# Performance work log

Measured on AMD Instinct MI355X. Metric: run time of the kernel, lower is better.

## Reference

```python
import jax, jax.numpy as jnp
import numpy as np
import math

B, SQ, SK, D = 32, 2048, 2048, 64


def setup_inputs() -> dict:
    key = jax.random.key(0)
    kq, kk, kv, km = jax.random.split(key, 4)
    Q = jax.random.normal(kq, (B, SQ, D), dtype=jnp.float32)
    K = jax.random.normal(kk, (B, SK, D), dtype=jnp.float32)
    V = jax.random.normal(kv, (B, SK, D), dtype=jnp.float32)
    mask = jax.random.randint(km, (B, SQ, SK), 0, 2) > 0  # bool, True = keep
    return {"Q": Q, "K": K, "V": V, "mask": mask}


def reference(Q, K, V, mask):
    dim_qk = Q.shape[-1]
    # [B, Sq, Sk] = Q @ K^T / sqrt(d)
    attn_score = jnp.einsum("bqd,bkd->bqk", Q, K) / math.sqrt(dim_qk)
    attn_score = jnp.where(mask, attn_score, jnp.float32(-1e9))
    attn_score = jax.nn.softmax(attn_score, axis=-1)
    output = jnp.einsum("bqk,bkd->bqd", attn_score, V)
    return (attn_score, output)
```

## Files before the change

kernel.cpp:

```cpp
#include <hip/hip_runtime.h>
#include <math.h>

#define NB 32
#define SQL 2048
#define SKL 2048
#define DH 64
#define EWP 40
#define SC 0.18033688011112042f

typedef __attribute__((ext_vector_type(8))) short short8;
typedef __attribute__((ext_vector_type(4))) float f32x4;
typedef __attribute__((ext_vector_type(4))) int   i32x4;
typedef __attribute__((ext_vector_type(2))) unsigned int u32x2;

__device__ __forceinline__ unsigned short f2bf(float f) {
    unsigned int u = __float_as_uint(f);
    u += 0x7FFFu + ((u >> 16) & 1u);
    return (unsigned short)(u >> 16);
}

__global__ __launch_bounds__(256)
void cvt_bf16_kernel(const float* __restrict__ in, unsigned short* __restrict__ out, int n4)
{
    const int i = blockIdx.x * 256 + threadIdx.x;
    if (i < n4) {
        const float4 v = reinterpret_cast<const float4*>(in)[i];
        ushort4 o;
        o.x = f2bf(v.x); o.y = f2bf(v.y); o.z = f2bf(v.z); o.w = f2bf(v.w);
        reinterpret_cast<ushort4*>(out)[i] = o;
    }
}

__global__ __launch_bounds__(256)
void vtrans_kernel(const float* __restrict__ V, unsigned short* __restrict__ Vt)
{
    __shared__ float tile[64][65];
    const int b  = blockIdx.x >> 5;
    const int kt = blockIdx.x & 31;
    const int t  = threadIdx.x;
    const int c4 = (t & 15) << 2;
    const int r0 = t >> 4;
    const float* vb = V + ((size_t)b * SKL + (size_t)kt * 64) * DH;
#pragma unroll
    for (int i = 0; i < 4; ++i) {
        const int r = r0 + i * 16;
        const float4 v = *reinterpret_cast<const float4*>(vb + (size_t)r * DH + c4);
        tile[r][c4] = v.x; tile[r][c4 + 1] = v.y; tile[r][c4 + 2] = v.z; tile[r][c4 + 3] = v.w;
    }
    __syncthreads();
    unsigned short* ob = Vt + (size_t)b * DH * SKL + (size_t)kt * 64;
#pragma unroll
    for (int i = 0; i < 4; ++i) {
        const int d = r0 + i * 16;
        ushort4 o;
        o.x = f2bf(tile[c4 + 0][d]);
        o.y = f2bf(tile[c4 + 1][d]);
        o.z = f2bf(tile[c4 + 2][d]);
        o.w = f2bf(tile[c4 + 3][d]);
        *reinterpret_cast<ushort4*>(ob + (size_t)d * SKL + c4) = o;
    }
}

__global__ __launch_bounds__(256, 6)
void sdpa_mfma_kernel(const unsigned short* __restrict__ Qb,
                      const unsigned short* __restrict__ Kb,
                      const unsigned short* __restrict__ Vtb,
                      const int* __restrict__ Mp,
                      float* __restrict__ Pout, float* __restrict__ Oout)
{
    __shared__ float ored[4][16][68];
    __shared__ float l_part[4][16];
    __shared__ float inv_l[16];

    const int tid  = threadIdx.x;
    const int w    = tid >> 6;
    const int lane = tid & 63;
    const int quad = lane >> 4;
    const int s    = lane & 15;
    const int b    = blockIdx.x >> 7;
    const int qt   = blockIdx.x & 127;
    const int g0   = (b << 11) + (qt << 4);

    const unsigned short* qrow = Qb + (size_t)(g0 + s) * DH + quad * 8;
    const short8 aq0 = *reinterpret_cast<const short8*>(qrow);
    const short8 aq1 = *reinterpret_cast<const short8*>(qrow + 32);

    const size_t kvb = (size_t)b * SKL * DH;
    const int* mrow = Mp + (size_t)(g0 + s) * SKL;

    unsigned int mregs[4] = {0u, 0u, 0u, 0u};
    float l_acc = 0.f;

#pragma unroll 1
    for (int it = 0; it < 4; ++it) {
#pragma unroll
        for (int o = 0; o < 4; ++o) {
            const int nt = it * 4 + o;
            const int j0 = nt * 128 + w * 32;
            const unsigned short* kb0 = Kb + kvb + (size_t)(j0 + s) * DH + quad * 8;
            const short8 k0a = *reinterpret_cast<const short8*>(kb0);
            const short8 k0b = *reinterpret_cast<const short8*>(kb0 + 32);
            const short8 k1a = *reinterpret_cast<const short8*>(kb0 + 16 * DH);
            const short8 k1b = *reinterpret_cast<const short8*>(kb0 + 16 * DH + 32);
            f32x4 c0 = {0.f, 0.f, 0.f, 0.f}, c1 = {0.f, 0.f, 0.f, 0.f};
            c0 = __builtin_amdgcn_mfma_f32_16x16x32_bf16(k0a, aq0, c0, 0, 0, 0);
            c0 = __builtin_amdgcn_mfma_f32_16x16x32_bf16(k0b, aq1, c0, 0, 0, 0);
            c1 = __builtin_amdgcn_mfma_f32_16x16x32_bf16(k1a, aq0, c1, 0, 0, 0);
            c1 = __builtin_amdgcn_mfma_f32_16x16x32_bf16(k1b, aq1, c1, 0, 0, 0);

            const i32x4 m0 = __builtin_nontemporal_load(
                reinterpret_cast<const i32x4*>(mrow + j0 + quad * 4));
            const i32x4 m1 = __builtin_nontemporal_load(
                reinterpret_cast<const i32x4*>(mrow + j0 + 16 + quad * 4));
            const unsigned int bits =
                (m0.x ? 1u : 0u)  | (m0.y ? 2u : 0u)  | (m0.z ? 4u : 0u)   | (m0.w ? 8u : 0u) |
                (m1.x ? 16u : 0u) | (m1.y ? 32u : 0u) | (m1.z ? 64u : 0u)  | (m1.w ? 128u : 0u);
            mregs[o] |= bits << (it * 8);

            float e;
            e = (bits & 1u)   ? exp2f(c0[0] * SC) : 0.f; l_acc += e;
            e = (bits & 2u)   ? exp2f(c0[1] * SC) : 0.f; l_acc += e;
            e = (bits & 4u)   ? exp2f(c0[2] * SC) : 0.f; l_acc += e;
            e = (bits & 8u)   ? exp2f(c0[3] * SC) : 0.f; l_acc += e;
            e = (bits & 16u)  ? exp2f(c1[0] * SC) : 0.f; l_acc += e;
            e = (bits & 32u)  ? exp2f(c1[1] * SC) : 0.f; l_acc += e;
            e = (bits & 64u)  ? exp2f(c1[2] * SC) : 0.f; l_acc += e;
            e = (bits & 128u) ? exp2f(c1[3] * SC) : 0.f; l_acc += e;
        }
    }

    l_acc += __shfl_xor(l_acc, 16, 64);
    l_acc += __shfl_xor(l_acc, 32, 64);
    if (lane < 16)
        l_part[w][lane] = l_acc;
    __syncthreads();
    if (tid < 16)
        inv_l[tid] = 1.0f / (l_part[0][tid] + l_part[1][tid] +
                             l_part[2][tid] + l_part[3][tid]);
    __syncthreads();
    const float il = inv_l[s];

    unsigned short* eW = reinterpret_cast<unsigned short*>(&ored[0][0][0]) + w * 2176;

    f32x4 o0 = {0.f, 0.f, 0.f, 0.f}, o1 = o0, o2 = o0, o3 = o0;
    const unsigned short* vrow = Vtb + (size_t)b * DH * SKL + (size_t)s * SKL;

#pragma unroll 1
    for (int it = 0; it < 4; ++it) {
#pragma unroll
        for (int o = 0; o < 4; ++o) {
            const int nt = it * 4 + o;
            const int j0 = nt * 128 + w * 32;
            const unsigned short* kb0 = Kb + kvb + (size_t)(j0 + s) * DH + quad * 8;
            const short8 k0a = *reinterpret_cast<const short8*>(kb0);
            const short8 k0b = *reinterpret_cast<const short8*>(kb0 + 32);
            const short8 k1a = *reinterpret_cast<const short8*>(kb0 + 16 * DH);
            const short8 k1b = *reinterpret_cast<const short8*>(kb0 + 16 * DH + 32);
            f32x4 c0 = {0.f, 0.f, 0.f, 0.f}, c1 = {0.f, 0.f, 0.f, 0.f};
            c0 = __builtin_amdgcn_mfma_f32_16x16x32_bf16(k0a, aq0, c0, 0, 0, 0);
            c0 = __builtin_amdgcn_mfma_f32_16x16x32_bf16(k0b, aq1, c0, 0, 0, 0);
            c1 = __builtin_amdgcn_mfma_f32_16x16x32_bf16(k1a, aq0, c1, 0, 0, 0);
            c1 = __builtin_amdgcn_mfma_f32_16x16x32_bf16(k1b, aq1, c1, 0, 0, 0);

            const unsigned int bits = mregs[o] >> (it * 8);
            const float e00 = (bits & 1u)   ? exp2f(c0[0] * SC) : 0.f;
            const float e01 = (bits & 2u)   ? exp2f(c0[1] * SC) : 0.f;
            const float e02 = (bits & 4u)   ? exp2f(c0[2] * SC) : 0.f;
            const float e03 = (bits & 8u)   ? exp2f(c0[3] * SC) : 0.f;
            const float e10 = (bits & 16u)  ? exp2f(c1[0] * SC) : 0.f;
            const float e11 = (bits & 32u)  ? exp2f(c1[1] * SC) : 0.f;
            const float e12 = (bits & 64u)  ? exp2f(c1[2] * SC) : 0.f;
            const float e13 = (bits & 128u) ? exp2f(c1[3] * SC) : 0.f;

            float* pb = Pout + (size_t)(g0 + s) * SKL + j0 + quad * 4;
            const f32x4 p0 = {e00 * il, e01 * il, e02 * il, e03 * il};
            const f32x4 p1 = {e10 * il, e11 * il, e12 * il, e13 * il};
            __builtin_nontemporal_store(p0, reinterpret_cast<f32x4*>(pb));
            __builtin_nontemporal_store(p1, reinterpret_cast<f32x4*>(pb + 16));

            u32x2 ev0, ev1;
            ev0.x = (unsigned)f2bf(e00) | ((unsigned)f2bf(e01) << 16);
            ev0.y = (unsigned)f2bf(e02) | ((unsigned)f2bf(e03) << 16);
            ev1.x = (unsigned)f2bf(e10) | ((unsigned)f2bf(e11) << 16);
            ev1.y = (unsigned)f2bf(e12) | ((unsigned)f2bf(e13) << 16);
            *reinterpret_cast<u32x2*>(eW + s * EWP + quad * 4) = ev0;
            *reinterpret_cast<u32x2*>(eW + s * EWP + 16 + quad * 4) = ev1;

            const short8 ap = *reinterpret_cast<const short8*>(eW + s * EWP + quad * 8);
            const unsigned short* vc = vrow + j0 + quad * 8;
            o0 = __builtin_amdgcn_mfma_f32_16x16x32_bf16(
                     ap, *reinterpret_cast<const short8*>(vc), o0, 0, 0, 0);
            o1 = __builtin_amdgcn_mfma_f32_16x16x32_bf16(
                     ap, *reinterpret_cast<const short8*>(vc + 16 * SKL), o1, 0, 0, 0);
            o2 = __builtin_amdgcn_mfma_f32_16x16x32_bf16(
                     ap, *reinterpret_cast<const short8*>(vc + 32 * SKL), o2, 0, 0, 0);
            o3 = __builtin_amdgcn_mfma_f32_16x16x32_bf16(
                     ap, *reinterpret_cast<const short8*>(vc + 48 * SKL), o3, 0, 0, 0);
        }
    }

#pragma unroll
    for (int r = 0; r < 4; ++r) {
        const int m = quad * 4 + r;
        ored[w][m][s]      = o0[r];
        ored[w][m][16 + s] = o1[r];
        ored[w][m][32 + s] = o2[r];
        ored[w][m][48 + s] = o3[r];
    }
    __syncthreads();
    {
        const int m  = tid >> 4;
        const int d4 = (tid & 15) << 2;
        const float* orp = &ored[0][m][d4];
        f32x4 a0 = *reinterpret_cast<const f32x4*>(orp);
        f32x4 a1 = *reinterpret_cast<const f32x4*>(orp + 16 * 68);
        f32x4 a2 = *reinterpret_cast<const f32x4*>(orp + 32 * 68);
        f32x4 a3 = *reinterpret_cast<const f32x4*>(orp + 48 * 68);
        f32x4 r = (a0 + a1) + (a2 + a3);
        const float ilm = inv_l[m];
        r[0] *= ilm; r[1] *= ilm; r[2] *= ilm; r[3] *= ilm;
        __builtin_nontemporal_store(r,
            reinterpret_cast<f32x4*>(Oout + (size_t)(g0 + m) * DH + d4));
    }
}

extern "C" void kernel_launch(void* const* d_in, const int* in_sizes, int n_in,
                              void* d_out, int out_size, void* d_ws, size_t ws_size,
                              hipStream_t stream) {
    const float* Q = (const float*)d_in[0];
    const float* K = (const float*)d_in[1];
    const float* V = (const float*)d_in[2];
    const int*   M = (const int*)d_in[3];

    float* Pout = (float*)d_out;
    float* Oout = Pout + (size_t)NB * SQL * SKL;

    unsigned short* Qb = (unsigned short*)d_ws;
    unsigned short* Kb = Qb + (size_t)NB * SQL * DH;
    unsigned short* Vt = Kb + (size_t)NB * SKL * DH;

    const int n4q = NB * SQL * DH / 4;
    cvt_bf16_kernel<<<n4q / 256, 256, 0, stream>>>(Q, Qb, n4q);
    cvt_bf16_kernel<<<n4q / 256, 256, 0, stream>>>(K, Kb, n4q);
    vtrans_kernel<<<NB * 32, 256, 0, stream>>>(V, Vt);

    const int blocks = NB * (SQL / 16);
    sdpa_mfma_kernel<<<blocks, 256, 0, stream>>>(Qb, Kb, Vt, M, Pout, Oout);
}
```

Measured before the change: 1.214 ms.

## Fuse two-pass softmax into single pass with register-held bf16 exponentials and 8 waves

Replaces the two-pass scheme, which recomputed QK^T and exp in a second pass, with one pass. Unnormalised exponentials are kept in registers as packed bf16 and used for both the row sum and the PV MFMA, then rescaled and written to the probability output after the row sum is known. The block grows to 512 threads (8 waves) so each wave covers only 8 key tiles. This removes the second QK^T and exp computation, but the stored probabilities now carry bf16 rounding, which may hurt accuracy, and register pressure rises.

```diff
diff --git a/kernel.cpp b/kernel.cpp
--- a/kernel.cpp
+++ b/kernel.cpp
@@ -17,6 +17,12 @@
     unsigned int u = __float_as_uint(f);
     u += 0x7FFFu + ((u >> 16) & 1u);
     return (unsigned short)(u >> 16);
+}
+__device__ __forceinline__ float bf_lo(unsigned int u) {
+    return __uint_as_float(u << 16);
+}
+__device__ __forceinline__ float bf_hi(unsigned int u) {
+    return __uint_as_float(u & 0xffff0000u);
 }
 
 __global__ __launch_bounds__(256)
@@ -61,15 +67,15 @@
     }
 }
 
-__global__ __launch_bounds__(256, 6)
+__global__ __launch_bounds__(512, 3)
 void sdpa_mfma_kernel(const unsigned short* __restrict__ Qb,
                       const unsigned short* __restrict__ Kb,
                       const unsigned short* __restrict__ Vtb,
                       const int* __restrict__ Mp,
                       float* __restrict__ Pout, float* __restrict__ Oout)
 {
-    __shared__ float ored[4][16][68];
-    __shared__ float l_part[4][16];
+    __shared__ float ored[8][16][68];
+    __shared__ float l_part[8][16];
     __shared__ float inv_l[16];
 
     const int tid  = threadIdx.x;
@@ -88,45 +94,61 @@
     const size_t kvb = (size_t)b * SKL * DH;
     const int* mrow = Mp + (size_t)(g0 + s) * SKL;
 
-    unsigned int mregs[4] = {0u, 0u, 0u, 0u};
+    unsigned short* eW = reinterpret_cast<unsigned short*>(&ored[0][0][0]) + w * 2176;
+    const unsigned short* vrow = Vtb + (size_t)b * DH * SKL + (size_t)s * SKL;
+
+    unsigned int E[8][4];
     float l_acc = 0.f;
-
-#pragma unroll 1
-    for (int it = 0; it < 4; ++it) {
-#pragma unroll
-        for (int o = 0; o < 4; ++o) {
-            const int nt = it * 4 + o;
-            const int j0 = nt * 128 + w * 32;
-            const unsigned short* kb0 = Kb + kvb + (size_t)(j0 + s) * DH + quad * 8;
-            const short8 k0a = *reinterpret_cast<const short8*>(kb0);
-            const short8 k0b = *reinterpret_cast<const short8*>(kb0 + 32);
-            const short8 k1a = *reinterpret_cast<const short8*>(kb0 + 16 * DH);
-            const short8 k1b = *reinterpret_cast<const short8*>(kb0 + 16 * DH + 32);
-            f32x4 c0 = {0.f, 0.f, 0.f, 0.f}, c1 = {0.f, 0.f, 0.f, 0.f};
-            c0 = __builtin_amdgcn_mfma_f32_16x16x32_bf16(k0a, aq0, c0, 0, 0, 0);
-            c0 = __builtin_amdgcn_mfma_f32_16x16x32_bf16(k0b, aq1, c0, 0, 0, 0);
-            c1 = __builtin_amdgcn_mfma_f32_16x16x32_bf16(k1a, aq0, c1, 0, 0, 0);
-            c1 = __builtin_amdgcn_mfma_f32_16x16x32_bf16(k1b, aq1, c1, 0, 0, 0);
-
-            const i32x4 m0 = __builtin_nontemporal_load(
-                reinterpret_cast<const i32x4*>(mrow + j0 + quad * 4));
-            const i32x4 m1 = __builtin_nontemporal_load(
-                reinterpret_cast<const i32x4*>(mrow + j0 + 16 + quad * 4));
-            const unsigned int bits =
-                (m0.x ? 1u : 0u)  | (m0.y ? 2u : 0u)  | (m0.z ? 4u : 0u)   | (m0.w ? 8u : 0u) |
-                (m1.x ? 16u : 0u) | (m1.y ? 32u : 0u) | (m1.z ? 64u : 0u)  | (m1.w ? 128u : 0u);
-            mregs[o] |= bits << (it * 8);
-
-            float e;
-            e = (bits & 1u)   ? exp2f(c0[0] * SC) : 0.f; l_acc += e;
-            e = (bits & 2u)   ? exp2f(c0[1] * SC) : 0.f; l_acc += e;
-            e = (bits & 4u)   ? exp2f(c0[2] * SC) : 0.f; l_acc += e;
-            e = (bits & 8u)   ? exp2f(c0[3] * SC) : 0.f; l_acc += e;
-            e = (bits & 16u)  ? exp2f(c1[0] * SC) : 0.f; l_acc += e;
-            e = (bits & 32u)  ? exp2f(c1[1] * SC) : 0.f; l_acc += e;
-            e = (bits & 64u)  ? exp2f(c1[2] * SC) : 0.f; l_acc += e;
-            e = (bits & 128u) ? exp2f(c1[3] * SC) : 0.f; l_acc += e;
-        }
+    f32x4 o0 = {0.f, 0.f, 0.f, 0.f}, o1 = o0, o2 = o0, o3 = o0;
+
+#pragma unroll
+    for (int nt = 0; nt < 8; ++nt) {
+        const int j0 = nt * 256 + w * 32;
+        const unsigned short* kb0 = Kb + kvb + (size_t)(j0 + s) * DH + quad * 8;
+        const short8 k0a = *reinterpret_cast<const short8*>(kb0);
+        const short8 k0b = *reinterpret_cast<const short8*>(kb0 + 32);
+        const short8 k1a = *reinterpret_cast<const short8*>(kb0 + 16 * DH);
+        const short8 k1b = *reinterpret_cast<const short8*>(kb0 + 16 * DH + 32);
+        f32x4 c0 = {0.f, 0.f, 0.f, 0.f}, c1 = {0.f, 0.f, 0.f, 0.f};
+        c0 = __builtin_amdgcn_mfma_f32_16x16x32_bf16(k0a, aq0, c0, 0, 0, 0);
+        c0 = __builtin_amdgcn_mfma_f32_16x16x32_bf16(k0b, aq1, c0, 0, 0, 0);
+        c1 = __builtin_amdgcn_mfma_f32_16x16x32_bf16(k1a, aq0, c1, 0, 0, 0);
+        c1 = __builtin_amdgcn_mfma_f32_16x16x32_bf16(k1b, aq1, c1, 0, 0, 0);
+
+        const i32x4 m0 = *reinterpret_cast<const i32x4*>(mrow + j0 + quad * 4);
+        const i32x4 m1 = *reinterpret_cast<const i32x4*>(mrow + j0 + 16 + quad * 4);
+
+        const float e00 = m0.x ? exp2f(c0[0] * SC) : 0.f;
+        const float e01 = m0.y ? exp2f(c0[1] * SC) : 0.f;
+        const float e02 = m0.z ? exp2f(c0[2] * SC) : 0.f;
+        const float e03 = m0.w ? exp2f(c0[3] * SC) : 0.f;
+        const float e10 = m1.x ? exp2f(c1[0] * SC) : 0.f;
+        const float e11 = m1.y ? exp2f(c1[1] * SC) : 0.f;
+        const float e12 = m1.z ? exp2f(c1[2] * SC) : 0.f;
+        const float e13 = m1.w ? exp2f(c1[3] * SC) : 0.f;
+        l_acc += ((e00 + e01) + (e02 + e03)) + ((e10 + e11) + (e12 + e13));
+
+        E[nt][0] = (unsigned)f2bf(e00) | ((unsigned)f2bf(e01) << 16);
+        E[nt][1] = (unsigned)f2bf(e02) | ((unsigned)f2bf(e03) << 16);
+        E[nt][2] = (unsigned)f2bf(e10) | ((unsigned)f2bf(e11) << 16);
+        E[nt][3] = (unsigned)f2bf(e12) | ((unsigned)f2bf(e13) << 16);
+
+        u32x2 ev0, ev1;
+        ev0.x = E[nt][0]; ev0.y = E[nt][1];
+        ev1.x = E[nt][2]; ev1.y = E[nt][3];
+        *reinterpret_cast<u32x2*>(eW + s * EWP + quad * 4) = ev0;
+        *reinterpret_cast<u32x2*>(eW + s * EWP + 16 + quad * 4) = ev1;
+
+        const short8 ap = *reinterpret_cast<const short8*>(eW + s * EWP + quad * 8);
+        const unsigned short* vc = vrow + j0 + quad * 8;
+        o0 = __builtin_amdgcn_mfma_f32_16x16x32_bf16(
+                 ap, *reinterpret_cast<const short8*>(vc), o0, 0, 0, 0);
+        o1 = __builtin_amdgcn_mfma_f32_16x16x32_bf16(
+                 ap, *reinterpret_cast<const short8*>(vc + 16 * SKL), o1, 0, 0, 0);
+        o2 = __builtin_amdgcn_mfma_f32_16x16x32_bf16(
+                 ap, *reinterpret_cast<const short8*>(vc + 32 * SKL), o2, 0, 0, 0);
+        o3 = __builtin_amdgcn_mfma_f32_16x16x32_bf16(
+                 ap, *reinterpret_cast<const short8*>(vc + 48 * SKL), o3, 0, 0, 0);
     }
 
     l_acc += __shfl_xor(l_acc, 16, 64);
@@ -134,70 +156,14 @@
     if (lane < 16)
         l_part[w][lane] = l_acc;
     __syncthreads();
-    if (tid < 16)
-        inv_l[tid] = 1.0f / (l_part[0][tid] + l_part[1][tid] +
-                             l_part[2][tid] + l_part[3][tid]);
+    if (tid < 16) {
+        float t = 0.f;
+#pragma unroll
+        for (int wv = 0; wv < 8; ++wv) t += l_part[wv][tid];
+        inv_l[tid] = 1.0f / t;
+    }
     __syncthreads();
     const float il = inv_l[s];
-
-    unsigned short* eW = reinterpret_cast<unsigned short*>(&ored[0][0][0]) + w * 2176;
-
-    f32x4 o0 = {0.f, 0.f, 0.f, 0.f}, o1 = o0, o2 = o0, o3 = o0;
-    const unsigned short* vrow = Vtb + (size_t)b * DH * SKL + (size_t)s * SKL;
-
-#pragma unroll 1
-    for (int it = 0; it < 4; ++it) {
-#pragma unroll
-        for (int o = 0; o < 4; ++o) {
-            const int nt = it * 4 + o;
-            const int j0 = nt * 128 + w * 32;
-            const unsigned short* kb0 = Kb + kvb + (size_t)(j0 + s) * DH + quad * 8;
-            const short8 k0a = *reinterpret_cast<const short8*>(kb0);
-            const short8 k0b = *reinterpret_cast<const short8*>(kb0 + 32);
-            const short8 k1a = *reinterpret_cast<const short8*>(kb0 + 16 * DH);
-            const short8 k1b = *reinterpret_cast<const short8*>(kb0 + 16 * DH + 32);
-            f32x4 c0 = {0.f, 0.f, 0.f, 0.f}, c1 = {0.f, 0.f, 0.f, 0.f};
-            c0 = __builtin_amdgcn_mfma_f32_16x16x32_bf16(k0a, aq0, c0, 0, 0, 0);
-            c0 = __builtin_amdgcn_mfma_f32_16x16x32_bf16(k0b, aq1, c0, 0, 0, 0);
-            c1 = __builtin_amdgcn_mfma_f32_16x16x32_bf16(k1a, aq0, c1, 0, 0, 0);
-            c1 = __builtin_amdgcn_mfma_f32_16x16x32_bf16(k1b, aq1, c1, 0, 0, 0);
-
-            const unsigned int bits = mregs[o] >> (it * 8);
-            const float e00 = (bits & 1u)   ? exp2f(c0[0] * SC) : 0.f;
-            const float e01 = (bits & 2u)   ? exp2f(c0[1] * SC) : 0.f;
-            const float e02 = (bits & 4u)   ? exp2f(c0[2] * SC) : 0.f;
-            const float e03 = (bits & 8u)   ? exp2f(c0[3] * SC) : 0.f;
-            const float e10 = (bits & 16u)  ? exp2f(c1[0] * SC) : 0.f;
-            const float e11 = (bits & 32u)  ? exp2f(c1[1] * SC) : 0.f;
-            const float e12 = (bits & 64u)  ? exp2f(c1[2] * SC) : 0.f;
-            const float e13 = (bits & 128u) ? exp2f(c1[3] * SC) : 0.f;
-
-            float* pb = Pout + (size_t)(g0 + s) * SKL + j0 + quad * 4;
-            const f32x4 p0 = {e00 * il, e01 * il, e02 * il, e03 * il};
-            const f32x4 p1 = {e10 * il, e11 * il, e12 * il, e13 * il};
-            __builtin_nontemporal_store(p0, reinterpret_cast<f32x4*>(pb));
-            __builtin_nontemporal_store(p1, reinterpret_cast<f32x4*>(pb + 16));
-
-            u32x2 ev0, ev1;
-            ev0.x = (unsigned)f2bf(e00) | ((unsigned)f2bf(e01) << 16);
-            ev0.y = (unsigned)f2bf(e02) | ((unsigned)f2bf(e03) << 16);
-            ev1.x = (unsigned)f2bf(e10) | ((unsigned)f2bf(e11) << 16);
-            ev1.y = (unsigned)f2bf(e12) | ((unsigned)f2bf(e13) << 16);
-            *reinterpret_cast<u32x2*>(eW + s * EWP + quad * 4) = ev0;
-            *reinterpret_cast<u32x2*>(eW + s * EWP + 16 + quad * 4) = ev1;
-
-            const short8 ap = *reinterpret_cast<const short8*>(eW + s * EWP + quad * 8);
-            const unsigned short* vc = vrow + j0 + quad * 8;
-            o0 = __builtin_amdgcn_mfma_f32_16x16x32_bf16(
-                     ap, *reinterpret_cast<const short8*>(vc), o0, 0, 0, 0);
-            o1 = __builtin_amdgcn_mfma_f32_16x16x32_bf16(
-                     ap, *reinterpret_cast<const short8*>(vc + 16 * SKL), o1, 0, 0, 0);
-            o2 = __builtin_amdgcn_mfma_f32_16x16x32_bf16(
-                     ap, *reinterpret_cast<const short8*>(vc + 32 * SKL), o2, 0, 0, 0);
-            o3 = __builtin_amdgcn_mfma_f32_16x16x32_bf16(
-                     ap, *reinterpret_cast<const short8*>(vc + 48 * SKL), o3, 0, 0, 0);
-        }
-    }
 
 #pragma unroll
     for (int r = 0; r < 4; ++r) {
@@ -208,19 +174,30 @@
         ored[w][m][48 + s] = o3[r];
     }
     __syncthreads();
-    {
+    if (tid < 256) {
         const int m  = tid >> 4;
         const int d4 = (tid & 15) << 2;
         const float* orp = &ored[0][m][d4];
-        f32x4 a0 = *reinterpret_cast<const f32x4*>(orp);
-        f32x4 a1 = *reinterpret_cast<const f32x4*>(orp + 16 * 68);
-        f32x4 a2 = *reinterpret_cast<const f32x4*>(orp + 32 * 68);
-        f32x4 a3 = *reinterpret_cast<const f32x4*>(orp + 48 * 68);
-        f32x4 r = (a0 + a1) + (a2 + a3);
+        f32x4 acc = *reinterpret_cast<const f32x4*>(orp);
+#pragma unroll
+        for (int wv = 1; wv < 8; ++wv)
+            acc += *reinterpret_cast<const f32x4*>(orp + (size_t)wv * 16 * 68);
         const float ilm = inv_l[m];
-        r[0] *= ilm; r[1] *= ilm; r[2] *= ilm; r[3] *= ilm;
-        __builtin_nontemporal_store(r,
-            reinterpret_cast<f32x4*>(Oout + (size_t)(g0 + m) * DH + d4));
+        acc[0] *= ilm; acc[1] *= ilm; acc[2] *= ilm; acc[3] *= ilm;
+        *reinterpret_cast<f32x4*>(Oout + (size_t)(g0 + m) * DH + d4) = acc;
+    }
+
+    float* pb = Pout + (size_t)(g0 + s) * SKL;
+#pragma unroll
+    for (int nt = 0; nt < 8; ++nt) {
+        const int j0 = nt * 256 + w * 32 + quad * 4;
+        f32x4 p0, p1;
+        p0[0] = bf_lo(E[nt][0]) * il; p0[1] = bf_hi(E[nt][0]) * il;
+        p0[2] = bf_lo(E[nt][1]) * il; p0[3] = bf_hi(E[nt][1]) * il;
+        p1[0] = bf_lo(E[nt][2]) * il; p1[1] = bf_hi(E[nt][2]) * il;
+        p1[2] = bf_lo(E[nt][3]) * il; p1[3] = bf_hi(E[nt][3]) * il;
+        *reinterpret_cast<f32x4*>(pb + j0)      = p0;
+        *reinterpret_cast<f32x4*>(pb + j0 + 16) = p1;
     }
 }
 
@@ -245,5 +222,5 @@
     vtrans_kernel<<<NB * 32, 256, 0, stream>>>(V, Vt);
 
     const int blocks = NB * (SQL / 16);
-    sdpa_mfma_kernel<<<blocks, 256, 0, stream>>>(Qb, Kb, Vt, M, Pout, Oout);
-}
+    sdpa_mfma_kernel<<<blocks, 512, 0, stream>>>(Qb, Kb, Vt, M, Pout, Oout);
+}
```

After: 1.200 ms. Within noise of the previous version (-1.1%).
